# Performance work log

Hardware: AMD Instinct MI355X
Metric: run time of the kernel (lower is better)

Reference implementation:

```python
import jax, jax.numpy as jnp
import numpy as np

B, L, D = 8, 2048, 1024

def setup_inputs() -> dict:
    key = jax.random.key(0)
    ks = jax.random.split(key, 12)
    s = 1.0 / np.sqrt(D)
    return {
        "q": jax.random.normal(ks[0], (B, L, D), jnp.float32),
        "k": jax.random.normal(ks[1], (B, L, D), jnp.float32),
        "v": jax.random.normal(ks[2], (B, L, D), jnp.float32),
        "mask": jnp.ones((B, L), jnp.float32),
        # Linear params stored as [in, out] so y = x @ W + b
        "Wq": jax.random.normal(ks[3], (D, D), jnp.float32) * s,
        "bq": jnp.zeros((D,), jnp.float32),
        "Wk": jax.random.normal(ks[4], (D, D), jnp.float32) * s,
        "bk": jnp.zeros((D,), jnp.float32),
        "Wv": jax.random.normal(ks[5], (D, D), jnp.float32) * s,
        "bv": jnp.zeros((D,), jnp.float32),
        "Wg": jax.random.normal(ks[6], (2 * D, D), jnp.float32) * (1.0 / np.sqrt(2 * D)),
        "bg": jnp.zeros((D,), jnp.float32),
    }

def reference(q, k, v, mask, Wq, bq, Wk, bk, Wv, bv, Wg, bg):
    q0 = q
    qp = q @ Wq + bq          # [B, Lq, D]
    kp = k @ Wk + bk          # [B, Lk, D]
    vp = v @ Wv + bv          # [B, Lk, D]
    scale = 1.0 / jnp.sqrt(jnp.asarray(qp.shape[-1], qp.dtype))
    w = jnp.einsum('bqd,bkd->bqk', qp, kp) * scale
    w = jax.nn.softmax(w, axis=-1)          # dim=2 == last axis for 3-D
    x = jnp.einsum('bqk,bkd->bqd', w, vp)
    gate = jnp.concatenate((qp, x), axis=-1) @ Wg + bg
    x = x * mask[..., None]
    x = x * jax.nn.sigmoid(gate)
    return x + q0  # add=True
```

## Files before the change

kernel.cpp:

```cpp
#include <hip/hip_runtime.h>

typedef unsigned int u32;
typedef unsigned short u16;
using v4f    = __attribute__((ext_vector_type(4))) float;
using short8 = __attribute__((ext_vector_type(8))) short;

#define GAS __attribute__((address_space(1)))
#define LAS __attribute__((address_space(3)))

__device__ __forceinline__ u16 f2bf(float f){
  u32 u = __builtin_bit_cast(u32, f);
  u32 r = (u + 0x7fffu + ((u >> 16) & 1u)) >> 16;
  return (u16)r;
}
__device__ __forceinline__ float bf2f(u16 h){
  u32 u = ((u32)h) << 16;
  return __builtin_bit_cast(float, u);
}

__device__ __forceinline__ void gld_lds16(const void* g, void* l){
  __builtin_amdgcn_global_load_lds((const GAS u32*)g, (LAS u32*)l, 16, 0, 0);
}

__global__ __launch_bounds__(256) void cvt_f32_bf16(
    const float* __restrict__ in, u16* __restrict__ out)
{
  const size_t i = ((size_t)blockIdx.x * 256 + threadIdx.x) * 8;
  v4f lo = *(const v4f*)(in + i);
  v4f hi = *(const v4f*)(in + i + 4);
  u32 p0 = (u32)f2bf(lo.x) | ((u32)f2bf(lo.y) << 16);
  u32 p1 = (u32)f2bf(lo.z) | ((u32)f2bf(lo.w) << 16);
  u32 p2 = (u32)f2bf(hi.x) | ((u32)f2bf(hi.y) << 16);
  u32 p3 = (u32)f2bf(hi.z) | ((u32)f2bf(hi.w) << 16);
  *(uint4*)(out + i) = make_uint4(p0, p1, p2, p3);
}

__global__ __launch_bounds__(256) void transpose_w_bf16(
    const float* __restrict__ in, u16* __restrict__ out, int K, int N)
{
  __shared__ float t[64][65];
  const int k0 = blockIdx.x * 64, n0 = blockIdx.y * 64;
  const int tx = threadIdx.x & 63, ty = threadIdx.x >> 6;
  #pragma unroll
  for (int i = 0; i < 16; i++){
    int r = ty + i * 4;
    t[r][tx] = in[(size_t)(k0 + r) * N + (n0 + tx)];
  }
  __syncthreads();
  #pragma unroll
  for (int i = 0; i < 16; i++){
    int r = ty + i * 4;
    out[(size_t)(n0 + r) * K + (k0 + tx)] = f2bf(t[tx][r]);
  }
}

__global__ __launch_bounds__(256) void softmax_rows(u16* __restrict__ S){
  const int lane = threadIdx.x & 63, wid = threadIdx.x >> 6;
  u16* p = S + ((size_t)blockIdx.x * 4 + wid) * 2048;
  uint4 u[4];
  #pragma unroll
  for (int j = 0; j < 4; j++) u[j] = ((const uint4*)p)[lane + j * 64];
  float f[32];
  #pragma unroll
  for (int j = 0; j < 4; j++){
    u32 w4[4] = {u[j].x, u[j].y, u[j].z, u[j].w};
    #pragma unroll
    for (int i = 0; i < 4; i++){
      f[j * 8 + 2*i]     = bf2f((u16)(w4[i] & 0xffffu));
      f[j * 8 + 2*i + 1] = bf2f((u16)(w4[i] >> 16));
    }
  }
  float m = f[0];
  #pragma unroll
  for (int i = 1; i < 32; i++) m = fmaxf(m, f[i]);
  #pragma unroll
  for (int o = 32; o >= 1; o >>= 1) m = fmaxf(m, __shfl_xor(m, o));
  float s = 0.f;
  #pragma unroll
  for (int i = 0; i < 32; i++){ f[i] = __expf(f[i] - m); s += f[i]; }
  #pragma unroll
  for (int o = 32; o >= 1; o >>= 1) s += __shfl_xor(s, o);
  const float inv = 1.f / s;
  #pragma unroll
  for (int j = 0; j < 4; j++){
    u32 w4[4];
    #pragma unroll
    for (int i = 0; i < 4; i++)
      w4[i] = (u32)f2bf(f[j * 8 + 2*i] * inv) |
              ((u32)f2bf(f[j * 8 + 2*i + 1] * inv) << 16);
    ((uint4*)p)[lane + j * 64] = make_uint4(w4[0], w4[1], w4[2], w4[3]);
  }
}

#define G256_BAR() do{ asm volatile("" ::: "memory");                       \
                       __builtin_amdgcn_s_barrier();                        \
                       asm volatile("" ::: "memory");                       \
                       __builtin_amdgcn_sched_barrier(0); }while(0)

#define G256_MFMA(NI0)                                                      \
    __builtin_amdgcn_s_setprio(1);                                          \
    _Pragma("unroll")                                                       \
    for (int mi = 0; mi < 8; mi++){                                         \
      acc[mi][NI0]     = __builtin_amdgcn_mfma_f32_16x16x32_bf16(           \
                           a[mi], b[0], acc[mi][NI0], 0, 0, 0);             \
      acc[mi][(NI0)+1] = __builtin_amdgcn_mfma_f32_16x16x32_bf16(           \
                           a[mi], b[1], acc[mi][(NI0)+1], 0, 0, 0);         \
    }                                                                       \
    __builtin_amdgcn_s_setprio(0);

template<int AMODE, int EPI>
__global__ __launch_bounds__(512, 2) void gemm256(
    const u16* __restrict__ Ab,
    const u16* __restrict__ A2b,
    const u16* __restrict__ BT,
    int lda, int ldb, int K,
    void* __restrict__ Cout, int ldc,
    const float* __restrict__ bias, float scale,
    size_t aBatch, size_t bBatch, size_t cBatch,
    const u16* __restrict__ xg,
    const float* __restrict__ maskp,
    const float* __restrict__ q0p)
{
  constexpr int BK = 64;
  __shared__ __align__(16) u16 As[2][2][128 * 64];
  __shared__ __align__(16) u16 Bs[2][2][128 * 64];

  const int z   = blockIdx.z;
  const int gx   = (int)gridDim.x;
  const int lin  = (int)blockIdx.y * gx + (int)blockIdx.x;
  const int l2gx = 31 - __clz(gx);
  const int g    = lin >> (3 + l2gx);
  const int rem  = lin & ((gx << 3) - 1);
  const int m0   = ((g << 3) + (rem & 7)) * 256;
  const int n0   = (rem >> 3) * 256;

  const int tid  = (int)threadIdx.x;
  const int lane = tid & 63, wid = tid >> 6;
  const int wm   = (wid >> 2) * 128;
  const int wn   = (wid & 3) * 64;
  const int wnh  = wn >> 7;
  const int wnl  = wn & 127;

  const u16* Az = Ab + (size_t)z * aBatch;
  const u16* Bz = BT + (size_t)z * bBatch;

  u32 offA[2][2], offB[2][2], ldsOffB[2];
  #pragma unroll
  for (int i = 0; i < 2; i++){
    int idx = tid + i * 512;
    int r = idx >> 3, c8 = idx & 7;
    int c8s = c8 ^ (r & 7);
    #pragma unroll
    for (int h = 0; h < 2; h++){
      offA[h][i] = (u32)(((m0 + h * 128 + r) * lda + c8s * 8) * 2);
      offB[h][i] = (u32)(((n0 + h * 128 + r) * ldb + c8s * 8) * 2);
    }
    ldsOffB[i] = (u32)(idx * 16);
  }

  auto stage = [&](int kt, int dbuf){
    const u16* Asrc; u32 ka;
    if (AMODE == 2){
      Asrc = (kt * BK < 1024) ? Az : A2b;
      ka = (u32)(((kt * BK) & 1023) * 2);
    } else {
      Asrc = Az;
      ka = (u32)(kt * BK * 2);
    }
    const u32 kb = (u32)(kt * BK * 2);
    #pragma unroll
    for (int h = 0; h < 2; h++){
      #pragma unroll
      for (int i = 0; i < 2; i++){
        gld_lds16((const char*)Asrc + offA[h][i] + ka,
                  (char*)&As[dbuf][h][0] + ldsOffB[i]);
        gld_lds16((const char*)Bz + offB[h][i] + kb,
                  (char*)&Bs[dbuf][h][0] + ldsOffB[i]);
      }
    }
  };

  v4f acc[8][4];
  #pragma unroll
  for (int mi = 0; mi < 8; mi++)
    #pragma unroll
    for (int ni = 0; ni < 4; ni++)
      acc[mi][ni] = (v4f){0.f, 0.f, 0.f, 0.f};

  const int ll  = lane & 15, lq = lane >> 4;
  const int ch0 = ((0 + lq) ^ (ll & 7)) << 3;
  const int ch4 = ((4 + lq) ^ (ll & 7)) << 3;

  stage(0, 0);
  const int nt = K / BK;
  for (int kt = 0; kt < nt; kt++){
    const int buf = kt & 1;
    if (kt + 1 < nt){
      stage(kt + 1, buf ^ 1);
      asm volatile("s_waitcnt vmcnt(8)" ::: "memory");
    } else {
      asm volatile("s_waitcnt vmcnt(0)" ::: "memory");
    }
    G256_BAR();

    const u16* aB = &As[buf][wid >> 2][0] + ll * 64;
    const u16* bB = &Bs[buf][wnh][0] + (wnl + ll) * 64;

    short8 a[8], b[2];
    b[0] = *(const short8*)(bB + ch0);
    b[1] = *(const short8*)(bB + ch0 + 1024);
    #pragma unroll
    for (int mi = 0; mi < 8; mi++) a[mi] = *(const short8*)(aB + ch0 + mi * 1024);
    G256_BAR();
    G256_MFMA(0)
    G256_BAR();
    b[0] = *(const short8*)(bB + ch0 + 2048);
    b[1] = *(const short8*)(bB + ch0 + 3072);
    G256_BAR();
    G256_MFMA(2)
    G256_BAR();
    b[0] = *(const short8*)(bB + ch4);
    b[1] = *(const short8*)(bB + ch4 + 1024);
    #pragma unroll
    for (int mi = 0; mi < 8; mi++) a[mi] = *(const short8*)(aB + ch4 + mi * 1024);
    G256_BAR();
    G256_MFMA(0)
    G256_BAR();
    b[0] = *(const short8*)(bB + ch4 + 2048);
    b[1] = *(const short8*)(bB + ch4 + 3072);
    G256_BAR();
    G256_MFMA(2)
    G256_BAR();
  }

  const int lr = lq * 4, lc = ll;
  if (EPI == 0 || EPI == 1){
    u16* C = (u16*)Cout + (size_t)z * cBatch;
    #pragma unroll
    for (int mi = 0; mi < 8; mi++){
      #pragma unroll
      for (int ni = 0; ni < 4; ni++){
        int col = n0 + wn + ni * 16 + lc;
        float bv = (EPI == 0) ? bias[col] : 0.f;
        #pragma unroll
        for (int r = 0; r < 4; r++){
          int row = m0 + wm + mi * 16 + lr + r;
          C[(size_t)row * ldc + col] = f2bf(acc[mi][ni][r] * scale + bv);
        }
      }
    }
  } else if (EPI == 3){
    u16* C = (u16*)Cout;
    #pragma unroll
    for (int mi = 0; mi < 8; mi++){
      int rowb = m0 + wm + mi * 16 + lr;
      int bb   = rowb >> 11;
      int rloc = rowb & 2047;
      #pragma unroll
      for (int ni = 0; ni < 4; ni++){
        int col = n0 + wn + ni * 16 + lc;
        float bv = bias[col];
        u32 pk0 = (u32)f2bf(acc[mi][ni][0] + bv) | ((u32)f2bf(acc[mi][ni][1] + bv) << 16);
        u32 pk1 = (u32)f2bf(acc[mi][ni][2] + bv) | ((u32)f2bf(acc[mi][ni][3] + bv) << 16);
        *(uint2*)&C[(size_t)bb * (1024ull * 2048) + (size_t)col * 2048 + rloc] =
            make_uint2(pk0, pk1);
      }
    }
  } else {
    float* C = (float*)Cout;
    #pragma unroll
    for (int mi = 0; mi < 8; mi++){
      #pragma unroll
      for (int ni = 0; ni < 4; ni++){
        int col = n0 + wn + ni * 16 + lc;
        float bv = bias[col];
        #pragma unroll
        for (int r = 0; r < 4; r++){
          int row = m0 + wm + mi * 16 + lr + r;
          float gg = acc[mi][ni][r] + bv;
          float sg = 1.f / (1.f + __expf(-gg));
          float xv = bf2f(xg[(size_t)row * 1024 + col]);
          C[(size_t)row * ldc + col] =
              xv * maskp[row] * sg + q0p[(size_t)row * 1024 + col];
        }
      }
    }
  }
}
#undef G256_BAR
#undef G256_MFMA

template<int AMODE, int EPI>
__global__ __launch_bounds__(256) void gemm128(
    const float* __restrict__ Af,
    const u16* __restrict__ Ab,
    const u16* __restrict__ A2b,
    const u16* __restrict__ BT,
    int lda, int ldb, int K,
    void* __restrict__ Cout, int ldc,
    const float* __restrict__ bias, float scale,
    size_t aBatch, size_t bBatch, size_t cBatch,
    const u16* __restrict__ xg,
    const float* __restrict__ maskp,
    const float* __restrict__ q0p)
{
  constexpr int BM = 128, BN = 128, BK = 64;
  __shared__ __align__(16) u16 As[BM * BK];
  __shared__ __align__(16) u16 Bs[BN * BK];
  const int z   = blockIdx.z;
  const int lin  = blockIdx.y * gridDim.x + blockIdx.x;
  const int l2gx = 31 - __clz((int)gridDim.x);
  const int g    = lin >> (3 + l2gx);
  const int rem  = lin & (((int)gridDim.x << 3) - 1);
  const int m0   = ((g << 3) + (rem & 7)) * BM;
  const int n0   = (rem >> 3) * BN;
  const int tid = threadIdx.x;
  const int lane = tid & 63, wid = tid >> 6;
  const int wm = (wid >> 1) * 64, wn = (wid & 1) * 64;
  const u16* Abz = Ab + (size_t)z * aBatch;
  const u16* BTz = BT + (size_t)z * bBatch;

  v4f acc[4][4];
  #pragma unroll
  for (int mi = 0; mi < 4; mi++)
    #pragma unroll
    for (int ni = 0; ni < 4; ni++)
      acc[mi][ni] = (v4f){0.f, 0.f, 0.f, 0.f};

  for (int k0 = 0; k0 < K; k0 += BK){
    if (AMODE == 0){
      #pragma unroll
      for (int i = 0; i < 4; i++){
        int idx = tid + i * 256;
        int r = idx >> 3, s = idx & 7;
        const float* src = Af + (size_t)(m0 + r) * lda + (k0 + s * 8);
        v4f lo = ((const v4f*)src)[0];
        v4f hi = ((const v4f*)src)[1];
        u32 p0 = (u32)f2bf(lo.x) | ((u32)f2bf(lo.y) << 16);
        u32 p1 = (u32)f2bf(lo.z) | ((u32)f2bf(lo.w) << 16);
        u32 p2 = (u32)f2bf(hi.x) | ((u32)f2bf(hi.y) << 16);
        u32 p3 = (u32)f2bf(hi.z) | ((u32)f2bf(hi.w) << 16);
        *(uint4*)&As[(size_t)idx * 8] = make_uint4(p0, p1, p2, p3);
      }
    } else {
      #pragma unroll
      for (int i = 0; i < 4; i++){
        int idx = tid + i * 256;
        int r = idx >> 3, s = idx & 7;
        int kk = k0 + s * 8;
        const u16* src;
        if (AMODE == 2){
          src = (kk < 1024) ? (Abz + (size_t)(m0 + r) * 1024 + kk)
                            : (A2b + (size_t)(m0 + r) * 1024 + (kk - 1024));
        } else {
          src = Abz + (size_t)(m0 + r) * lda + kk;
        }
        gld_lds16(src, &As[(size_t)idx * 8]);
      }
    }
    #pragma unroll
    for (int i = 0; i < 4; i++){
      int idx = tid + i * 256;
      int r = idx >> 3, s = idx & 7;
      gld_lds16(BTz + (size_t)(n0 + r) * ldb + (k0 + s * 8), &Bs[(size_t)idx * 8]);
    }
    __syncthreads();
    #pragma unroll
    for (int ks = 0; ks < BK; ks += 32){
      short8 a[4], b[4];
      #pragma unroll
      for (int mi = 0; mi < 4; mi++)
        a[mi] = *(const short8*)&As[(wm + mi * 16 + (lane & 15)) * BK + ks + (lane >> 4) * 8];
      #pragma unroll
      for (int ni = 0; ni < 4; ni++)
        b[ni] = *(const short8*)&Bs[(wn + ni * 16 + (lane & 15)) * BK + ks + (lane >> 4) * 8];
      #pragma unroll
      for (int mi = 0; mi < 4; mi++)
        #pragma unroll
        for (int ni = 0; ni < 4; ni++)
          acc[mi][ni] = __builtin_amdgcn_mfma_f32_16x16x32_bf16(a[mi], b[ni], acc[mi][ni], 0, 0, 0);
    }
    __syncthreads();
  }

  const int lr = (lane >> 4) * 4, lc = lane & 15;
  if (EPI == 0 || EPI == 1){
    u16* C = (u16*)Cout + (size_t)z * cBatch;
    #pragma unroll
    for (int mi = 0; mi < 4; mi++){
      #pragma unroll
      for (int ni = 0; ni < 4; ni++){
        int col = n0 + wn + ni * 16 + lc;
        float bv = (EPI == 0) ? bias[col] : 0.f;
        #pragma unroll
        for (int r = 0; r < 4; r++){
          int row = m0 + wm + mi * 16 + lr + r;
          C[(size_t)row * ldc + col] = f2bf(acc[mi][ni][r] * scale + bv);
        }
      }
    }
  } else if (EPI == 3){
    u16* C = (u16*)Cout;
    #pragma unroll
    for (int mi = 0; mi < 4; mi++){
      int rowb = m0 + wm + mi * 16 + lr;
      int b    = rowb >> 11;
      int rloc = rowb & 2047;
      #pragma unroll
      for (int ni = 0; ni < 4; ni++){
        int col = n0 + wn + ni * 16 + lc;
        float bv = bias[col];
        u32 pk[2];
        pk[0] = (u32)f2bf(acc[mi][ni][0] + bv) | ((u32)f2bf(acc[mi][ni][1] + bv) << 16);
        pk[1] = (u32)f2bf(acc[mi][ni][2] + bv) | ((u32)f2bf(acc[mi][ni][3] + bv) << 16);
        *(uint2*)&C[(size_t)b * (1024ull * 2048) + (size_t)col * 2048 + rloc] =
            make_uint2(pk[0], pk[1]);
      }
    }
  } else {
    float* C = (float*)Cout;
    #pragma unroll
    for (int mi = 0; mi < 4; mi++){
      #pragma unroll
      for (int ni = 0; ni < 4; ni++){
        int col = n0 + wn + ni * 16 + lc;
        float bv = bias[col];
        #pragma unroll
        for (int r = 0; r < 4; r++){
          int row = m0 + wm + mi * 16 + lr + r;
          float g  = acc[mi][ni][r] + bv;
          float sg = 1.f / (1.f + __expf(-g));
          float xv = bf2f(xg[(size_t)row * 1024 + col]);
          C[(size_t)row * ldc + col] =
              xv * maskp[row] * sg + q0p[(size_t)row * 1024 + col];
        }
      }
    }
  }
}

extern "C" void kernel_launch(void* const* d_in, const int* in_sizes, int n_in,
                              void* d_out, int out_size, void* d_ws, size_t ws_size,
                              hipStream_t stream)
{
  const float* q    = (const float*)d_in[0];
  const float* k    = (const float*)d_in[1];
  const float* v    = (const float*)d_in[2];
  const float* mask = (const float*)d_in[3];
  const float* Wq   = (const float*)d_in[4];
  const float* bq   = (const float*)d_in[5];
  const float* Wk   = (const float*)d_in[6];
  const float* bk   = (const float*)d_in[7];
  const float* Wv   = (const float*)d_in[8];
  const float* bv   = (const float*)d_in[9];
  const float* Wg   = (const float*)d_in[10];
  const float* bg   = (const float*)d_in[11];
  float* out = (float*)d_out;

  char* ws = (char*)d_ws;
  const size_t MB = 1024ull * 1024ull;
  u16* WqT = (u16*)(ws + 0 * MB);
  u16* WkT = (u16*)(ws + 2 * MB);
  u16* WvT = (u16*)(ws + 4 * MB);
  u16* WgT = (u16*)(ws + 6 * MB);
  u16* qp  = (u16*)(ws + 10 * MB);
  u16* kp  = (u16*)(ws + 42 * MB);
  u16* vpT = (u16*)(ws + 74 * MB);
  u16* S   = (u16*)(ws + 106 * MB);
  u16* tmp = (u16*)(ws + 106 * MB);
  u16* x   = kp;

  const bool bigws = ws_size >= 138 * MB;
  int nb = 8;
  while (nb > 1 && 106 * MB + (size_t)nb * 8 * MB > ws_size) nb >>= 1;
  const int nchunks = 8 / nb;

  dim3 B(256);
  dim3 T5(512);

  transpose_w_bf16<<<dim3(16, 16, 1), B, 0, stream>>>(Wq, WqT, 1024, 1024);
  transpose_w_bf16<<<dim3(16, 16, 1), B, 0, stream>>>(Wk, WkT, 1024, 1024);
  transpose_w_bf16<<<dim3(16, 16, 1), B, 0, stream>>>(Wv, WvT, 1024, 1024);
  transpose_w_bf16<<<dim3(32, 16, 1), B, 0, stream>>>(Wg, WgT, 2048, 1024);

  if (bigws){
    cvt_f32_bf16<<<dim3(8192), B, 0, stream>>>(q, tmp);
    gemm256<1, 0><<<dim3(4, 64, 1), T5, 0, stream>>>(tmp, nullptr, WqT,
        1024, 1024, 1024, qp, 1024, bq, 1.f, 0, 0, 0, nullptr, nullptr, nullptr);
    cvt_f32_bf16<<<dim3(8192), B, 0, stream>>>(k, tmp);
    gemm256<1, 0><<<dim3(4, 64, 1), T5, 0, stream>>>(tmp, nullptr, WkT,
        1024, 1024, 1024, kp, 1024, bk, 1.f, 0, 0, 0, nullptr, nullptr, nullptr);
    cvt_f32_bf16<<<dim3(8192), B, 0, stream>>>(v, tmp);
    gemm256<1, 3><<<dim3(4, 64, 1), T5, 0, stream>>>(tmp, nullptr, WvT,
        1024, 1024, 1024, vpT, 0, bv, 1.f, 0, 0, 0, nullptr, nullptr, nullptr);

    for (int c = 0; c < nchunks; c++){
      const size_t boff = (size_t)c * nb;
      gemm256<1, 1><<<dim3(8, 8, nb), T5, 0, stream>>>(
          qp + boff * 2048 * 1024, nullptr, kp + boff * 2048 * 1024,
          1024, 1024, 1024, S, 2048, nullptr, 0.03125f,
          2048ull * 1024, 2048ull * 1024, 2048ull * 2048, nullptr, nullptr, nullptr);
      softmax_rows<<<dim3(nb * 512, 1, 1), B, 0, stream>>>(S);
      gemm256<1, 1><<<dim3(4, 8, nb), T5, 0, stream>>>(
          S, nullptr, vpT + boff * 1024 * 2048,
          2048, 2048, 2048, x + boff * 2048 * 1024, 1024, nullptr, 1.f,
          2048ull * 2048, 1024ull * 2048, 2048ull * 1024, nullptr, nullptr, nullptr);
    }

    gemm256<2, 2><<<dim3(4, 64, 1), T5, 0, stream>>>(qp, x, WgT,
        1024, 2048, 2048, out, 1024, bg, 1.f, 0, 0, 0, x, mask, q);
  } else {
    gemm128<0, 0><<<dim3(8, 128, 1), B, 0, stream>>>(q, nullptr, nullptr, WqT,
        1024, 1024, 1024, qp, 1024, bq, 1.f, 0, 0, 0, nullptr, nullptr, nullptr);
    gemm128<0, 0><<<dim3(8, 128, 1), B, 0, stream>>>(k, nullptr, nullptr, WkT,
        1024, 1024, 1024, kp, 1024, bk, 1.f, 0, 0, 0, nullptr, nullptr, nullptr);
    gemm128<0, 3><<<dim3(8, 128, 1), B, 0, stream>>>(v, nullptr, nullptr, WvT,
        1024, 1024, 1024, vpT, 0, bv, 1.f, 0, 0, 0, nullptr, nullptr, nullptr);

    for (int c = 0; c < nchunks; c++){
      const size_t boff = (size_t)c * nb;
      gemm128<1, 1><<<dim3(16, 16, nb), B, 0, stream>>>(nullptr,
          qp + boff * 2048 * 1024, nullptr, kp + boff * 2048 * 1024,
          1024, 1024, 1024, S, 2048, nullptr, 0.03125f,
          2048ull * 1024, 2048ull * 1024, 2048ull * 2048, nullptr, nullptr, nullptr);
      softmax_rows<<<dim3(nb * 512, 1, 1), B, 0, stream>>>(S);
      gemm128<1, 1><<<dim3(8, 16, nb), B, 0, stream>>>(nullptr,
          S, nullptr, vpT + boff * 1024 * 2048,
          2048, 2048, 2048, x + boff * 2048 * 1024, 1024, nullptr, 1.f,
          2048ull * 2048, 1024ull * 2048, 2048ull * 1024, nullptr, nullptr, nullptr);
    }

    gemm128<2, 2><<<dim3(8, 128, 1), B, 0, stream>>>(nullptr, qp, x, WgT,
        1024, 2048, 2048, out, 1024, bg, 1.f, 0, 0, 0, x, mask, q);
  }
}
```

Baseline: 703.8 us.

## Remove per-phase workgroup barriers in gemm256 and prefetch B fragments ahead of MFMAs

Replaces the many s_barrier calls between each LDS-read and MFMA phase of the gemm256 main loop with two barriers per k-tile: one after an lgkmcnt wait before restaging, and one after the global-load wait. B fragments for later MFMA groups are loaded into separate registers ahead of time so LDS reads overlap with MFMA execution. The goal is to cut barrier stalls and let waves interleave LDS and matrix work more freely, at the cost of more VGPR pressure under a 512x2 launch bound.

Result: faster. 643.0 us (-8.6%).

```diff
diff --git a/kernel.cpp b/kernel.cpp
--- a/kernel.cpp
+++ b/kernel.cpp
@@ -92,19 +92,14 @@
   }
 }
 
-#define G256_BAR() do{ asm volatile("" ::: "memory");                       \
-                       __builtin_amdgcn_s_barrier();                        \
-                       asm volatile("" ::: "memory");                       \
-                       __builtin_amdgcn_sched_barrier(0); }while(0)
-
-#define G256_MFMA(NI0)                                                      \
+#define MFMA8(B0, B1, N0, N1)                                               \
     __builtin_amdgcn_s_setprio(1);                                          \
     _Pragma("unroll")                                                       \
     for (int mi = 0; mi < 8; mi++){                                         \
-      acc[mi][NI0]     = __builtin_amdgcn_mfma_f32_16x16x32_bf16(           \
-                           a[mi], b[0], acc[mi][NI0], 0, 0, 0);             \
-      acc[mi][(NI0)+1] = __builtin_amdgcn_mfma_f32_16x16x32_bf16(           \
-                           a[mi], b[1], acc[mi][(NI0)+1], 0, 0, 0);         \
+      acc[mi][N0] = __builtin_amdgcn_mfma_f32_16x16x32_bf16(                \
+                      a[mi], (B0), acc[mi][N0], 0, 0, 0);                   \
+      acc[mi][N1] = __builtin_amdgcn_mfma_f32_16x16x32_bf16(                \
+                      a[mi], (B1), acc[mi][N1], 0, 0, 0);                   \
     }                                                                       \
     __builtin_amdgcn_s_setprio(0);
 
@@ -195,42 +190,42 @@
   const int nt = K / BK;
   for (int kt = 0; kt < nt; kt++){
     const int buf = kt & 1;
+
+    asm volatile("s_waitcnt lgkmcnt(0)" ::: "memory");
+    __builtin_amdgcn_sched_barrier(0);
+    __builtin_amdgcn_s_barrier();
+    asm volatile("" ::: "memory");
     if (kt + 1 < nt){
       stage(kt + 1, buf ^ 1);
       asm volatile("s_waitcnt vmcnt(8)" ::: "memory");
     } else {
       asm volatile("s_waitcnt vmcnt(0)" ::: "memory");
     }
-    G256_BAR();
+    __builtin_amdgcn_s_barrier();
+    asm volatile("" ::: "memory");
+    __builtin_amdgcn_sched_barrier(0);
 
     const u16* aB = &As[buf][wid >> 2][0] + ll * 64;
     const u16* bB = &Bs[buf][wnh][0] + (wnl + ll) * 64;
 
-    short8 a[8], b[2];
-    b[0] = *(const short8*)(bB + ch0);
-    b[1] = *(const short8*)(bB + ch0 + 1024);
+    short8 a[8], b0[2], b1[2], p0[2], p1[2];
+    b0[0] = *(const short8*)(bB + ch0);
+    b0[1] = *(const short8*)(bB + ch0 + 1024);
     #pragma unroll
     for (int mi = 0; mi < 8; mi++) a[mi] = *(const short8*)(aB + ch0 + mi * 1024);
-    G256_BAR();
-    G256_MFMA(0)
-    G256_BAR();
-    b[0] = *(const short8*)(bB + ch0 + 2048);
-    b[1] = *(const short8*)(bB + ch0 + 3072);
-    G256_BAR();
-    G256_MFMA(2)
-    G256_BAR();
-    b[0] = *(const short8*)(bB + ch4);
-    b[1] = *(const short8*)(bB + ch4 + 1024);
+    b1[0] = *(const short8*)(bB + ch0 + 2048);
+    b1[1] = *(const short8*)(bB + ch0 + 3072);
+    MFMA8(b0[0], b0[1], 0, 1)
+    p0[0] = *(const short8*)(bB + ch4);
+    p0[1] = *(const short8*)(bB + ch4 + 1024);
+    MFMA8(b1[0], b1[1], 2, 3)
+    p1[0] = *(const short8*)(bB + ch4 + 2048);
+    p1[1] = *(const short8*)(bB + ch4 + 3072);
+    __builtin_amdgcn_sched_barrier(0);
     #pragma unroll
     for (int mi = 0; mi < 8; mi++) a[mi] = *(const short8*)(aB + ch4 + mi * 1024);
-    G256_BAR();
-    G256_MFMA(0)
-    G256_BAR();
-    b[0] = *(const short8*)(bB + ch4 + 2048);
-    b[1] = *(const short8*)(bB + ch4 + 3072);
-    G256_BAR();
-    G256_MFMA(2)
-    G256_BAR();
+    MFMA8(p0[0], p0[1], 0, 1)
+    MFMA8(p1[0], p1[1], 2, 3)
   }
 
   const int lr = lq * 4, lc = ll;
@@ -287,8 +282,7 @@
     }
   }
 }
-#undef G256_BAR
-#undef G256_MFMA
+#undef MFMA8
 
 template<int AMODE, int EPI>
 __global__ __launch_bounds__(256) void gemm128(
```
